# Kernel tuning notes

Hardware: AMD Instinct MI355X
Metric: run time of the kernel (lower is better)

The kernel has to match this reference:

```python
import jax, jax.numpy as jnp
import numpy as np

BS, C_IN, H, W = 16, 128, 64, 64
C_OUT, K, STRIDE, PAD, DIL = 256, 3, 1, 1, 1
ALPHA = 0.5  # scaling_factor
QMAX = 127.0  # int8 symmetric fake-quant


def _fake_quant(t):
    # symmetric per-tensor int8 fake quantization with straight-through estimator
    s = jax.lax.stop_gradient(jnp.max(jnp.abs(t))) / QMAX
    s = jnp.where(s == 0, 1.0, s)
    q = jnp.clip(jnp.round(t / s), -QMAX, QMAX) * s
    return t + jax.lax.stop_gradient(q - t)  # STE


def setup_inputs() -> dict:
    key = jax.random.key(0)
    k1, k2, k3 = jax.random.split(key, 3)
    x = jax.random.normal(k1, (BS, C_IN, H, W), dtype=jnp.float32)
    weight = jax.random.normal(k2, (C_OUT, C_IN, K, K), dtype=jnp.float32) * 0.05
    bias = jax.random.normal(k3, (C_OUT,), dtype=jnp.float32) * 0.01
    return {"x": x, "weight": weight, "bias": bias}


def reference(x, weight, bias):
    bs, _, h_in, w_in = x.shape
    ickhkw = C_IN * K * K
    h_out = (h_in + 2 * PAD - DIL * (K - 1) - 1) // STRIDE + 1
    w_out = (w_in + 2 * PAD - DIL * (K - 1) - 1) // STRIDE + 1

    # im2col (matches torch F.unfold feature ordering: channel-major, then kh, kw)
    patches = jax.lax.conv_general_dilated_patches(
        x, filter_shape=(K, K), window_strides=(STRIDE, STRIDE),
        padding=((PAD, PAD), (PAD, PAD)), rhs_dilation=(DIL, DIL),
    )  # [bs, ickhkw, h_out, w_out]
    cols = patches.reshape(bs, ickhkw, h_out * w_out)
    cols = cols.transpose(0, 2, 1).reshape(-1, ickhkw)  # [bs*L, ickhkw]

    w2 = weight.reshape(C_OUT, ickhkw)

    # SmoothQuant per-column scales (detached)
    w_scale = jax.lax.stop_gradient(jnp.max(jnp.abs(w2), axis=0))    # [ickhkw]
    act_scale = jax.lax.stop_gradient(jnp.max(jnp.abs(cols), axis=0))  # [ickhkw]
    scale = act_scale ** ALPHA / w_scale ** (1.0 - ALPHA)
    scale = jnp.where(scale == 0, 1.0, scale)

    w_s = _fake_quant(w2 * scale)
    x_s = _fake_quant(cols / scale)

    out = x_s @ w_s.T  # [bs*L, C_OUT]
    out = out.reshape(bs, h_out * w_out, C_OUT).transpose(0, 2, 1)
    out = out.reshape(bs, C_OUT, h_out, w_out)
    return out + bias.reshape(1, C_OUT, 1, 1)
```

## Files before the change

### kernel.cpp

```cpp
#include <hip/hip_runtime.h>
#include <cstdint>

#define C_IN   128
#define C_OUT  256
#define KK     1152
#define NPIX   4096
#define BS     16
#define M_ROWS 65536
#define QMAXF  127.0f

typedef int v4i __attribute__((ext_vector_type(4)));

#define OFF_WPART 0
#define OFF_QW    75497472
#define OFF_SCALE 75792384
#define OFF_QMUL  75796992
#define OFF_APART 75801600
#define OFF_SCAL  75843072

__global__ void k_prep(const float* __restrict__ x, const float* __restrict__ wgt,
                       float* __restrict__ act_part, float* __restrict__ w_part) {
    const int tid = threadIdx.x;
    if (blockIdx.x >= 1024) {
        int t = blockIdx.x - 1024;
        int j = (t % 5) * 256 + tid;
        int s = t / 5;
        if (j >= KK) return;
        const float* p = wgt + (size_t)s * 16 * KK + j;
        float m = 0.f;
#pragma unroll
        for (int i = 0; i < 16; i++) m = fmaxf(m, fabsf(p[(size_t)i * KK]));
        w_part[s * KK + j] = m;
        return;
    }
    const int c = blockIdx.x >> 3, s = blockIdx.x & 7;
    float m[9];
#pragma unroll
    for (int i = 0; i < 9; i++) m[i] = 0.f;
    const float4* xp4 = (const float4*)(x + (size_t)(s * 2) * (C_IN * NPIX) + (size_t)c * NPIX);
    const int img4 = C_IN * NPIX / 4;
    for (int v = tid; v < 2048; v += 256) {
        int half = v >> 10;
        int hw4  = v & 1023;
        int h   = hw4 >> 4;
        int w4i = hw4 & 15;
        float4 f = xp4[half * img4 + hw4];
        float ax = fabsf(f.x), ay = fabsf(f.y), az = fabsf(f.z), aw = fabsf(f.w);
        float vall = fmaxf(fmaxf(ax, ay), fmaxf(az, aw));
        float vnoF = (w4i == 0)  ? fmaxf(fmaxf(ay, az), aw) : vall;
        float vnoL = (w4i == 15) ? fmaxf(fmaxf(ax, ay), az) : vall;
        bool r0 = (h <= 62), r2 = (h >= 1);
        m[0] = fmaxf(m[0], r0 ? vnoL : 0.f);
        m[1] = fmaxf(m[1], r0 ? vall : 0.f);
        m[2] = fmaxf(m[2], r0 ? vnoF : 0.f);
        m[3] = fmaxf(m[3], vnoL);
        m[4] = fmaxf(m[4], vall);
        m[5] = fmaxf(m[5], vnoF);
        m[6] = fmaxf(m[6], r2 ? vnoL : 0.f);
        m[7] = fmaxf(m[7], r2 ? vall : 0.f);
        m[8] = fmaxf(m[8], r2 ? vnoF : 0.f);
    }
    __shared__ float sm[9][4];
    int lane = tid & 63, wid = tid >> 6;
#pragma unroll
    for (int i = 0; i < 9; i++) {
        float v = m[i];
        for (int off = 32; off > 0; off >>= 1) v = fmaxf(v, __shfl_down(v, off));
        if (lane == 0) sm[i][wid] = v;
    }
    __syncthreads();
    if (tid < 9) {
        float v = fmaxf(fmaxf(sm[tid][0], sm[tid][1]), fmaxf(sm[tid][2], sm[tid][3]));
        act_part[s * KK + c * 9 + tid] = v;
    }
}

__global__ void k_scalequant(const float* __restrict__ act_part, const float* __restrict__ w_part,
                             const float* __restrict__ wgt,
                             float* __restrict__ qmul, float* __restrict__ scalars,
                             signed char* __restrict__ qWp) {
    const int tid = threadIdx.x;
    __shared__ float ssc[KK];
    __shared__ float red[16];
    __shared__ float s_sw, s_sx;
    float mx = 0.f, mw = 0.f;
    for (int j = tid; j < KK; j += 256) {
        float a = 0.f;
#pragma unroll
        for (int s = 0; s < 8; s++) a = fmaxf(a, act_part[s * KK + j]);
        float wv = 0.f;
#pragma unroll
        for (int s = 0; s < 16; s++) wv = fmaxf(wv, w_part[s * KK + j]);
        float sc = sqrtf(a) / sqrtf(wv);
        if (sc == 0.f) sc = 1.0f;
        ssc[j] = sc;
        mx = fmaxf(mx, a / sc);
        mw = fmaxf(mw, wv * sc);
    }
    int lane = tid & 63, wid = tid >> 6;
    for (int off = 32; off > 0; off >>= 1) {
        mx = fmaxf(mx, __shfl_down(mx, off));
        mw = fmaxf(mw, __shfl_down(mw, off));
    }
    if (lane == 0) { red[wid] = mx; red[8 + wid] = mw; }
    __syncthreads();
    if (tid == 0) {
        float a = fmaxf(fmaxf(red[0], red[1]), fmaxf(red[2], red[3]));
        float b = fmaxf(fmaxf(red[8], red[9]), fmaxf(red[10], red[11]));
        float s_x = a / QMAXF; if (s_x == 0.f) s_x = 1.f;
        float s_w = b / QMAXF; if (s_w == 0.f) s_w = 1.f;
        s_sx = s_x; s_sw = s_w;
    }
    __syncthreads();
    const int bid = blockIdx.x;
    if (bid == 0) {
        const float s_x = s_sx, s_w = s_sw;
        if (tid == 0) { scalars[0] = s_x; scalars[1] = s_w; scalars[2] = s_x * s_w; }
        for (int j = tid; j < KK; j += 256) qmul[j] = 1.0f / (ssc[j] * s_x);
        return;
    }
    const int m = bid - 1;
    const float s_w = s_sw;
    for (int kp = tid; kp < KK; kp += 256) {
        int tap = kp >> 7, c = kp & 127;
        int j = c * 9 + tap;
        float t = wgt[(size_t)m * KK + j] * ssc[j];
        float q = rintf(t / s_w);
        q = fminf(fmaxf(q, -QMAXF), QMAXF);
        qWp[(size_t)m * KK + kp] = (signed char)(int)q;
    }
}

__global__ __launch_bounds__(512, 4) void k_gemm(const signed char* __restrict__ qWp,
                                                 const float* __restrict__ x,
                                                 const float* __restrict__ qmul,
                                                 const float* __restrict__ scalars,
                                                 const float* __restrict__ bias,
                                                 float* __restrict__ out) {
    __shared__ __align__(16) signed char Bs[2][64 * 128];
    __shared__ float qm[KK];
    const int tid = threadIdx.x;
    const int lane = tid & 63, wv = tid >> 6;
    const int bid = blockIdx.x;
    const int swz = (bid & 7) * 128 + (bid >> 3);
    const int b  = swz >> 6;
    const int oh = swz & 63;
    const float* xb = x + (size_t)b * (C_IN * NPIX);
    const int c0 = wv * 16;

    for (int i = tid; i < KK; i += 512) {
        int tap = i >> 7, c = i & 127;
        qm[i] = qmul[c * 9 + tap];
    }

    const signed char* aBase = qWp + (size_t)(wv * 32 + (lane & 15)) * KK + (lane >> 4) * 16;

    v4i acc[2][4];
#pragma unroll
    for (int i = 0; i < 2; i++)
#pragma unroll
        for (int jq = 0; jq < 4; jq++) acc[i][jq] = (v4i){0, 0, 0, 0};

    float xr[16], xrn[16];
    {
        const bool ok = oh >= 1;
        const float* s = xb + (oh - 1) * 64 + lane;
#pragma unroll
        for (int d = 0; d < 16; d++) xr[d] = ok ? s[(size_t)(c0 + d) * NPIX] : 0.f;
    }
    v4i af[2][2], afn[2][2];
#pragma unroll
    for (int h = 0; h < 2; h++)
#pragma unroll
        for (int mt = 0; mt < 2; mt++)
            af[h][mt] = *(const v4i*)(aBase + (size_t)mt * 16 * KK + 0 * 128 + h * 64);

    __syncthreads();

#pragma unroll
    for (int tap = 0; tap < 9; tap++) {
        const int g  = (tap * 11) >> 5;
        const int jj = tap - g * 3;
        const int s  = jj - 1;
        signed char* bsp = (signed char*)Bs[tap & 1];

        {
            int n = lane - s;
            bool valid = (unsigned)n < 64u;
            int wrow = valid ? n : (s == -1 ? 0 : 63);
            const float* qmt = qm + tap * 128 + c0;
            int pk[4];
#pragma unroll
            for (int d4 = 0; d4 < 4; d4++) {
                int q0 = (int)rintf(xr[d4 * 4 + 0] * qmt[d4 * 4 + 0]);
                int q1 = (int)rintf(xr[d4 * 4 + 1] * qmt[d4 * 4 + 1]);
                int q2 = (int)rintf(xr[d4 * 4 + 2] * qmt[d4 * 4 + 2]);
                int q3 = (int)rintf(xr[d4 * 4 + 3] * qmt[d4 * 4 + 3]);
                unsigned t0 = __builtin_amdgcn_perm((unsigned)q1, (unsigned)q0, 0x0c0c0400u);
                unsigned t1 = __builtin_amdgcn_perm((unsigned)q3, (unsigned)q2, 0x0c0c0400u);
                int w = (int)__builtin_amdgcn_perm(t1, t0, 0x05040100u);
                pk[d4] = valid ? w : 0;
            }
            *(v4i*)(bsp + wrow * 128 + ((wv ^ (wrow & 7)) * 16)) = (v4i){pk[0], pk[1], pk[2], pk[3]};
        }

        if (jj == 0 && g < 2) {
            const bool ok = (unsigned)(oh + g) < 64u;
            const float* sp = xb + (oh + g) * 64 + lane;
#pragma unroll
            for (int d = 0; d < 16; d++) xrn[d] = ok ? sp[(size_t)(c0 + d) * NPIX] : 0.f;
        }

        __syncthreads();

        if (tap < 8) {
#pragma unroll
            for (int h = 0; h < 2; h++)
#pragma unroll
                for (int mt = 0; mt < 2; mt++)
                    afn[h][mt] = *(const v4i*)(aBase + (size_t)mt * 16 * KK + (tap + 1) * 128 + h * 64);
        }

#pragma unroll
        for (int h = 0; h < 2; h++) {
            const int q4 = h * 4 + (lane >> 4);
            v4i bf[4];
#pragma unroll
            for (int nt = 0; nt < 4; nt++) {
                int rb = nt * 16 + (lane & 15);
                bf[nt] = *(const v4i*)(bsp + rb * 128 + ((q4 ^ (rb & 7)) * 16));
            }
#pragma unroll
            for (int mt = 0; mt < 2; mt++)
#pragma unroll
                for (int nt = 0; nt < 4; nt++)
                    acc[mt][nt] = __builtin_amdgcn_mfma_i32_16x16x64_i8(af[h][mt], bf[nt], acc[mt][nt], 0, 0, 0);
        }

        if (tap < 8) {
#pragma unroll
            for (int h = 0; h < 2; h++)
#pragma unroll
                for (int mt = 0; mt < 2; mt++) af[h][mt] = afn[h][mt];
        }
        if (jj == 2 && g < 2) {
#pragma unroll
            for (int d = 0; d < 16; d++) xr[d] = xrn[d];
        }
    }

    const float ssp = scalars[2];
    const int quad = lane >> 4, col = lane & 15;
    float bv[2][4];
#pragma unroll
    for (int mt = 0; mt < 2; mt++)
#pragma unroll
        for (int rg = 0; rg < 4; rg++)
            bv[mt][rg] = bias[wv * 32 + mt * 16 + quad * 4 + rg];

    float* obase = out + ((size_t)b * C_OUT) * NPIX + oh * 64;
#pragma unroll
    for (int mt = 0; mt < 2; mt++) {
#pragma unroll
        for (int nt = 0; nt < 4; nt++) {
            int n = nt * 16 + col;
#pragma unroll
            for (int rg = 0; rg < 4; rg++) {
                int m = wv * 32 + mt * 16 + quad * 4 + rg;
                obase[(size_t)m * NPIX + n] = (float)acc[mt][nt][rg] * ssp + bv[mt][rg];
            }
        }
    }
}

extern "C" void kernel_launch(void* const* d_in, const int* in_sizes, int n_in,
                              void* d_out, int out_size, void* d_ws, size_t ws_size,
                              hipStream_t stream) {
    const float* x    = (const float*)d_in[0];
    const float* wgt  = (const float*)d_in[1];
    const float* bias = (const float*)d_in[2];
    float* out = (float*)d_out;

    char* ws = (char*)d_ws;
    float* w_part    = (float*)(ws + OFF_WPART);
    signed char* qWp = (signed char*)(ws + OFF_QW);
    float* qmul      = (float*)(ws + OFF_QMUL);
    float* act_part  = (float*)(ws + OFF_APART);
    float* scalars   = (float*)(ws + OFF_SCAL);

    k_prep<<<1104, 256, 0, stream>>>(x, wgt, act_part, w_part);
    k_scalequant<<<257, 256, 0, stream>>>(act_part, w_part, wgt, qmul, scalars, qWp);
    k_gemm<<<BS * 64, 512, 0, stream>>>(qWp, x, qmul, scalars, bias, out);
}
```

Measured before the change: 142.6 us.

## Fuse prep, scale-quant and GEMM into one cooperative kernel with grid syncs

Replaces the three kernel launches with a single cooperative kernel of 512 persistent blocks. Grid-wide barriers separate the stages: per-column absmax, scale and weight quantisation, then the int8 MFMA GEMM. Every block recomputes the scales redundantly, and each block handles two output rows in the GEMM phase. This removes launch gaps and workspace round-trips, but it adds grid-sync cost and halves the GEMM grid, which may reduce latency hiding. The old three-kernel path stays as a fallback if the cooperative launch fails.

```diff
diff --git a/kernel.cpp b/kernel.cpp
--- a/kernel.cpp
+++ b/kernel.cpp
@@ -1,12 +1,14 @@
 #include <hip/hip_runtime.h>
+#include <hip/hip_cooperative_groups.h>
 #include <cstdint>
+
+namespace cg = cooperative_groups;
 
 #define C_IN   128
 #define C_OUT  256
 #define KK     1152
 #define NPIX   4096
 #define BS     16
-#define M_ROWS 65536
 #define QMAXF  127.0f
 
 typedef int v4i __attribute__((ext_vector_type(4)));
@@ -17,6 +19,258 @@
 #define OFF_QMUL  75796992
 #define OFF_APART 75801600
 #define OFF_SCAL  75843072
+
+__global__ __launch_bounds__(512, 4) void k_all(const float* __restrict__ x,
+                                                const float* __restrict__ wgt,
+                                                const float* __restrict__ bias,
+                                                float* __restrict__ out,
+                                                float* __restrict__ act_part,
+                                                float* __restrict__ w_part,
+                                                signed char* __restrict__ qWp) {
+    cg::grid_group grid = cg::this_grid();
+    __shared__ __align__(16) signed char Bs[2][64 * 128];
+    __shared__ float qm[KK];
+    __shared__ float sm[9][8];
+    __shared__ float red[16];
+    __shared__ float s_sx_sh, s_sw_sh;
+
+    const int tid = threadIdx.x;
+    const int lane = tid & 63, wv = tid >> 6;
+    const int bid = blockIdx.x;
+
+    const int img4 = C_IN * NPIX / 4;
+#pragma unroll 1
+    for (int pp = 0; pp < 2; ++pp) {
+        const int p = bid + pp * 512;
+        const int c = p >> 3, s = p & 7;
+        float m[9];
+#pragma unroll
+        for (int i = 0; i < 9; i++) m[i] = 0.f;
+        const float4* xp4 = (const float4*)(x + (size_t)(s * 2) * (C_IN * NPIX) + (size_t)c * NPIX);
+        for (int v = tid; v < 2048; v += 512) {
+            int half = v >> 10;
+            int hw4  = v & 1023;
+            int h   = hw4 >> 4;
+            int w4i = hw4 & 15;
+            float4 f = xp4[half * img4 + hw4];
+            float ax = fabsf(f.x), ay = fabsf(f.y), az = fabsf(f.z), aw = fabsf(f.w);
+            float vall = fmaxf(fmaxf(ax, ay), fmaxf(az, aw));
+            float vnoF = (w4i == 0)  ? fmaxf(fmaxf(ay, az), aw) : vall;
+            float vnoL = (w4i == 15) ? fmaxf(fmaxf(ax, ay), az) : vall;
+            bool r0 = (h <= 62), r2 = (h >= 1);
+            m[0] = fmaxf(m[0], r0 ? vnoL : 0.f);
+            m[1] = fmaxf(m[1], r0 ? vall : 0.f);
+            m[2] = fmaxf(m[2], r0 ? vnoF : 0.f);
+            m[3] = fmaxf(m[3], vnoL);
+            m[4] = fmaxf(m[4], vall);
+            m[5] = fmaxf(m[5], vnoF);
+            m[6] = fmaxf(m[6], r2 ? vnoL : 0.f);
+            m[7] = fmaxf(m[7], r2 ? vall : 0.f);
+            m[8] = fmaxf(m[8], r2 ? vnoF : 0.f);
+        }
+#pragma unroll
+        for (int i = 0; i < 9; i++) {
+            float v = m[i];
+            for (int off = 32; off > 0; off >>= 1) v = fmaxf(v, __shfl_down(v, off));
+            if (lane == 0) sm[i][wv] = v;
+        }
+        __syncthreads();
+        if (tid < 9) {
+            float v = sm[tid][0];
+#pragma unroll
+            for (int i = 1; i < 8; i++) v = fmaxf(v, sm[tid][i]);
+            act_part[s * KK + c * 9 + tid] = v;
+        }
+        __syncthreads();
+    }
+    if (bid >= 476) {
+        int u = (bid - 476) * 512 + tid;
+        int s = u / 1152;
+        int j = u - s * 1152;
+        const float* pw = wgt + (size_t)s * 16 * KK + j;
+        float mW = 0.f;
+#pragma unroll
+        for (int i = 0; i < 16; i++) mW = fmaxf(mW, fabsf(pw[(size_t)i * KK]));
+        w_part[s * KK + j] = mW;
+    }
+    grid.sync();
+
+    float mx = 0.f, mwp = 0.f;
+    for (int j = tid; j < KK; j += 512) {
+        float a = 0.f;
+#pragma unroll
+        for (int s = 0; s < 8; s++) a = fmaxf(a, act_part[s * KK + j]);
+        float wvv = 0.f;
+#pragma unroll
+        for (int s = 0; s < 16; s++) wvv = fmaxf(wvv, w_part[s * KK + j]);
+        float sc = sqrtf(a) / sqrtf(wvv);
+        if (sc == 0.f) sc = 1.0f;
+        int c = j / 9, tap = j - c * 9;
+        qm[tap * 128 + c] = sc;
+        mx  = fmaxf(mx, a / sc);
+        mwp = fmaxf(mwp, wvv * sc);
+    }
+    for (int off = 32; off > 0; off >>= 1) {
+        mx  = fmaxf(mx,  __shfl_down(mx, off));
+        mwp = fmaxf(mwp, __shfl_down(mwp, off));
+    }
+    if (lane == 0) { red[wv] = mx; red[8 + wv] = mwp; }
+    __syncthreads();
+    if (tid == 0) {
+        float a = red[0], b = red[8];
+#pragma unroll
+        for (int i = 1; i < 8; i++) { a = fmaxf(a, red[i]); b = fmaxf(b, red[8 + i]); }
+        float s_x = a / QMAXF; if (s_x == 0.f) s_x = 1.f;
+        float s_w = b / QMAXF; if (s_w == 0.f) s_w = 1.f;
+        s_sx_sh = s_x; s_sw_sh = s_w;
+    }
+    __syncthreads();
+    const float s_x = s_sx_sh, s_w = s_sw_sh;
+    if (bid < 256) {
+        const float* wrow = wgt + (size_t)bid * KK;
+        signed char* qrow = qWp + (size_t)bid * KK;
+        for (int kp = tid; kp < KK; kp += 512) {
+            int tap = kp >> 7, c = kp & 127;
+            int j = c * 9 + tap;
+            float t = wrow[j] * qm[kp];
+            float q = rintf(t / s_w);
+            q = fminf(fmaxf(q, -QMAXF), QMAXF);
+            qrow[kp] = (signed char)(int)q;
+        }
+    }
+    __syncthreads();
+    for (int idx = tid; idx < KK; idx += 512) qm[idx] = 1.0f / (qm[idx] * s_x);
+    const float ssp = s_x * s_w;
+    grid.sync();
+
+    const int c0 = wv * 16;
+    const signed char* aBase = qWp + (size_t)(wv * 32 + (lane & 15)) * KK + (lane >> 4) * 16;
+    const int quad = lane >> 4, col = lane & 15;
+    float bv[2][4];
+#pragma unroll
+    for (int mt = 0; mt < 2; mt++)
+#pragma unroll
+        for (int rg = 0; rg < 4; rg++)
+            bv[mt][rg] = bias[wv * 32 + mt * 16 + quad * 4 + rg];
+
+    const int swzb = (bid & 7) * 64 + (bid >> 3);
+
+#pragma unroll 1
+    for (int it = 0; it < 2; ++it) {
+        const int tile = swzb * 2 + it;
+        const int b  = tile >> 6;
+        const int oh = tile & 63;
+        const float* xb = x + (size_t)b * (C_IN * NPIX);
+
+        v4i acc[2][4];
+#pragma unroll
+        for (int i = 0; i < 2; i++)
+#pragma unroll
+            for (int jq = 0; jq < 4; jq++) acc[i][jq] = (v4i){0, 0, 0, 0};
+
+        float xr[16], xrn[16];
+        {
+            const bool ok = oh >= 1;
+            const float* sp = xb + (oh - 1) * 64 + lane;
+#pragma unroll
+            for (int d = 0; d < 16; d++) xr[d] = ok ? sp[(size_t)(c0 + d) * NPIX] : 0.f;
+        }
+        v4i af[2][2], afn[2][2];
+#pragma unroll
+        for (int h = 0; h < 2; h++)
+#pragma unroll
+            for (int mt = 0; mt < 2; mt++)
+                af[h][mt] = *(const v4i*)(aBase + (size_t)mt * 16 * KK + 0 * 128 + h * 64);
+
+        __syncthreads();
+
+#pragma unroll
+        for (int tap = 0; tap < 9; tap++) {
+            const int g  = (tap * 11) >> 5;
+            const int jj = tap - g * 3;
+            const int s  = jj - 1;
+            signed char* bsp = (signed char*)Bs[tap & 1];
+
+            {
+                int n = lane - s;
+                bool valid = (unsigned)n < 64u;
+                int wrow = valid ? n : (s == -1 ? 0 : 63);
+                const float* qmt = qm + tap * 128 + c0;
+                int pk[4];
+#pragma unroll
+                for (int d4 = 0; d4 < 4; d4++) {
+                    int q0 = (int)rintf(xr[d4 * 4 + 0] * qmt[d4 * 4 + 0]);
+                    int q1 = (int)rintf(xr[d4 * 4 + 1] * qmt[d4 * 4 + 1]);
+                    int q2 = (int)rintf(xr[d4 * 4 + 2] * qmt[d4 * 4 + 2]);
+                    int q3 = (int)rintf(xr[d4 * 4 + 3] * qmt[d4 * 4 + 3]);
+                    unsigned t0 = __builtin_amdgcn_perm((unsigned)q1, (unsigned)q0, 0x0c0c0400u);
+                    unsigned t1 = __builtin_amdgcn_perm((unsigned)q3, (unsigned)q2, 0x0c0c0400u);
+                    int w = (int)__builtin_amdgcn_perm(t1, t0, 0x05040100u);
+                    pk[d4] = valid ? w : 0;
+                }
+                *(v4i*)(bsp + wrow * 128 + ((wv ^ (wrow & 7)) * 16)) = (v4i){pk[0], pk[1], pk[2], pk[3]};
+            }
+
+            if (jj == 0 && g < 2) {
+                const bool ok = (unsigned)(oh + g) < 64u;
+                const float* sp = xb + (oh + g) * 64 + lane;
+#pragma unroll
+                for (int d = 0; d < 16; d++) xrn[d] = ok ? sp[(size_t)(c0 + d) * NPIX] : 0.f;
+            }
+
+            __syncthreads();
+
+            if (tap < 8) {
+#pragma unroll
+                for (int h = 0; h < 2; h++)
+#pragma unroll
+                    for (int mt = 0; mt < 2; mt++)
+                        afn[h][mt] = *(const v4i*)(aBase + (size_t)mt * 16 * KK + (tap + 1) * 128 + h * 64);
+            }
+
+#pragma unroll
+            for (int h = 0; h < 2; h++) {
+                const int q4 = h * 4 + (lane >> 4);
+                v4i bf[4];
+#pragma unroll
+                for (int nt = 0; nt < 4; nt++) {
+                    int rb = nt * 16 + (lane & 15);
+                    bf[nt] = *(const v4i*)(bsp + rb * 128 + ((q4 ^ (rb & 7)) * 16));
+                }
+#pragma unroll
+                for (int mt = 0; mt < 2; mt++)
+#pragma unroll
+                    for (int nt = 0; nt < 4; nt++)
+                        acc[mt][nt] = __builtin_amdgcn_mfma_i32_16x16x64_i8(af[h][mt], bf[nt], acc[mt][nt], 0, 0, 0);
+            }
+
+            if (tap < 8) {
+#pragma unroll
+                for (int h = 0; h < 2; h++)
+#pragma unroll
+                    for (int mt = 0; mt < 2; mt++) af[h][mt] = afn[h][mt];
+            }
+            if (jj == 2 && g < 2) {
+#pragma unroll
+                for (int d = 0; d < 16; d++) xr[d] = xrn[d];
+            }
+        }
+
+        float* obase = out + ((size_t)b * C_OUT) * NPIX + oh * 64;
+#pragma unroll
+        for (int mt = 0; mt < 2; mt++) {
+#pragma unroll
+            for (int nt = 0; nt < 4; nt++) {
+                int n = nt * 16 + col;
+#pragma unroll
+                for (int rg = 0; rg < 4; rg++) {
+                    int m = wv * 32 + mt * 16 + quad * 4 + rg;
+                    obase[(size_t)m * NPIX + n] = (float)acc[mt][nt][rg] * ssp + bv[mt][rg];
+                }
+            }
+        }
+    }
+}
 
 __global__ void k_prep(const float* __restrict__ x, const float* __restrict__ wgt,
                        float* __restrict__ act_part, float* __restrict__ w_part) {
@@ -152,15 +406,12 @@
         int tap = i >> 7, c = i & 127;
         qm[i] = qmul[c * 9 + tap];
     }
-
     const signed char* aBase = qWp + (size_t)(wv * 32 + (lane & 15)) * KK + (lane >> 4) * 16;
-
     v4i acc[2][4];
 #pragma unroll
     for (int i = 0; i < 2; i++)
 #pragma unroll
         for (int jq = 0; jq < 4; jq++) acc[i][jq] = (v4i){0, 0, 0, 0};
-
     float xr[16], xrn[16];
     {
         const bool ok = oh >= 1;
@@ -174,16 +425,13 @@
 #pragma unroll
         for (int mt = 0; mt < 2; mt++)
             af[h][mt] = *(const v4i*)(aBase + (size_t)mt * 16 * KK + 0 * 128 + h * 64);
-
-    __syncthreads();
-
+    __syncthreads();
 #pragma unroll
     for (int tap = 0; tap < 9; tap++) {
         const int g  = (tap * 11) >> 5;
         const int jj = tap - g * 3;
         const int s  = jj - 1;
         signed char* bsp = (signed char*)Bs[tap & 1];
-
         {
             int n = lane - s;
             bool valid = (unsigned)n < 64u;
@@ -203,16 +451,13 @@
             }
             *(v4i*)(bsp + wrow * 128 + ((wv ^ (wrow & 7)) * 16)) = (v4i){pk[0], pk[1], pk[2], pk[3]};
         }
-
         if (jj == 0 && g < 2) {
             const bool ok = (unsigned)(oh + g) < 64u;
             const float* sp = xb + (oh + g) * 64 + lane;
 #pragma unroll
             for (int d = 0; d < 16; d++) xrn[d] = ok ? sp[(size_t)(c0 + d) * NPIX] : 0.f;
         }
-
         __syncthreads();
-
         if (tap < 8) {
 #pragma unroll
             for (int h = 0; h < 2; h++)
@@ -220,7 +465,6 @@
                 for (int mt = 0; mt < 2; mt++)
                     afn[h][mt] = *(const v4i*)(aBase + (size_t)mt * 16 * KK + (tap + 1) * 128 + h * 64);
         }
-
 #pragma unroll
         for (int h = 0; h < 2; h++) {
             const int q4 = h * 4 + (lane >> 4);
@@ -236,7 +480,6 @@
                 for (int nt = 0; nt < 4; nt++)
                     acc[mt][nt] = __builtin_amdgcn_mfma_i32_16x16x64_i8(af[h][mt], bf[nt], acc[mt][nt], 0, 0, 0);
         }
-
         if (tap < 8) {
 #pragma unroll
             for (int h = 0; h < 2; h++)
@@ -248,7 +491,6 @@
             for (int d = 0; d < 16; d++) xr[d] = xrn[d];
         }
     }
-
     const float ssp = scalars[2];
     const int quad = lane >> 4, col = lane & 15;
     float bv[2][4];
@@ -257,7 +499,6 @@
 #pragma unroll
         for (int rg = 0; rg < 4; rg++)
             bv[mt][rg] = bias[wv * 32 + mt * 16 + quad * 4 + rg];
-
     float* obase = out + ((size_t)b * C_OUT) * NPIX + oh * 64;
 #pragma unroll
     for (int mt = 0; mt < 2; mt++) {
@@ -288,7 +529,13 @@
     float* act_part  = (float*)(ws + OFF_APART);
     float* scalars   = (float*)(ws + OFF_SCAL);
 
-    k_prep<<<1104, 256, 0, stream>>>(x, wgt, act_part, w_part);
-    k_scalequant<<<257, 256, 0, stream>>>(act_part, w_part, wgt, qmul, scalars, qWp);
-    k_gemm<<<BS * 64, 512, 0, stream>>>(qWp, x, qmul, scalars, bias, out);
+    void* kargs[] = { (void*)&x, (void*)&wgt, (void*)&bias, (void*)&out,
+                      (void*)&act_part, (void*)&w_part, (void*)&qWp };
+    hipError_t e = hipLaunchCooperativeKernel((const void*)k_all, dim3(512), dim3(512),
+                                              kargs, 0, stream);
+    if (e != hipSuccess) {
+        k_prep<<<1104, 256, 0, stream>>>(x, wgt, act_part, w_part);
+        k_scalequant<<<257, 256, 0, stream>>>(act_part, w_part, wgt, qmul, scalars, qWp);
+        k_gemm<<<BS * 64, 512, 0, stream>>>(qWp, x, qmul, scalars, bias, out);
+    }
 }
```

After: 265.3 us. 1.86x slower.
